# Performance work log

Measured on AMD Instinct MI355X. Metric: run time of the kernel, lower is better.

Reference implementation:

```python
import math
import jax, jax.numpy as jnp
import numpy as np

BS = 4; C = 128; D = 128; NH = 4; NL = 2; NP = 8
SHAPES = [(64, 96), (32, 48)]            # (H, W) per level
STARTS = [0, SHAPES[0][0] * SHAPES[0][1]]  # level_start_index


def lrelu(x):
    return jnp.where(x >= 0, x, 0.1 * x)


def conv2d(x, w, b):
    y = jax.lax.conv_general_dilated(x, w, (1, 1), [(1, 1), (1, 1)],
                                     dimension_numbers=('NCHW', 'OIHW', 'NCHW'))
    return y + b[None, :, None, None]


def pos_enc_sine(bs, H, W, npf=64, T=10000.0):
    # DETR PositionEmbeddingSine (normalize=True), mask of ones -> cumsum = index+1
    scale = 2.0 * math.pi
    eps = 1e-6
    y = (jnp.arange(1, H + 1, dtype=jnp.float32) / (H + eps) * scale)[:, None]
    x = (jnp.arange(1, W + 1, dtype=jnp.float32) / (W + eps) * scale)[None, :]
    y = jnp.broadcast_to(y, (H, W))
    x = jnp.broadcast_to(x, (H, W))
    dim_t = T ** (2.0 * (jnp.arange(npf) // 2).astype(jnp.float32) / npf)
    px = x[..., None] / dim_t
    py = y[..., None] / dim_t
    def interleave(p):
        return jnp.stack([jnp.sin(p[..., 0::2]), jnp.cos(p[..., 1::2])], -1).reshape(H, W, npf)
    pos = jnp.concatenate([interleave(py), interleave(px)], -1)  # [H,W,2*npf]
    return jnp.broadcast_to(pos.transpose(2, 0, 1)[None], (bs, 2 * npf, H, W))


def ref_points(bs, H, W):
    ys = (jnp.arange(H, dtype=jnp.float32) + 0.5) / H
    xs = (jnp.arange(W, dtype=jnp.float32) + 0.5) / W
    gy, gx = jnp.meshgrid(ys, xs, indexing='ij')
    ref = jnp.stack([gx.reshape(-1), gy.reshape(-1)], -1)  # [hw, 2] (x, y)
    return jnp.broadcast_to(ref[None, :, None, :], (bs, H * W, 1, 2))


def sample_level(v, loc, Hl, Wl):
    # v: [bs, Hl*Wl, nh, d]; loc: [bs, nq, nh, np, 2] in [0,1] -> grid_sample bilinear, zero pad
    bs, nq, nh, npts, _ = loc.shape
    d = v.shape[-1]
    x = loc[..., 0] * Wl - 0.5
    y = loc[..., 1] * Hl - 0.5
    x0f = jnp.floor(x); y0f = jnp.floor(y)
    fx = x - x0f; fy = y - y0f
    x0 = x0f.astype(jnp.int32); y0 = y0f.astype(jnp.int32)
    def gather(xi, yi):
        valid = (xi >= 0) & (xi < Wl) & (yi >= 0) & (yi < Hl)
        idx = jnp.clip(yi, 0, Hl - 1) * Wl + jnp.clip(xi, 0, Wl - 1)  # [bs,nq,nh,np]
        idx = idx.transpose(0, 1, 3, 2).reshape(bs, nq * npts, nh)
        g = jnp.take_along_axis(v, idx[..., None], axis=1)  # [bs,nq*np,nh,d]
        g = g.reshape(bs, nq, npts, nh, d).transpose(0, 1, 3, 2, 4)  # [bs,nq,nh,np,d]
        return g * valid[..., None]
    w00 = (1 - fx) * (1 - fy); w01 = fx * (1 - fy); w10 = (1 - fx) * fy; w11 = fx * fy
    return (gather(x0, y0) * w00[..., None] + gather(x0 + 1, y0) * w01[..., None]
            + gather(x0, y0 + 1) * w10[..., None] + gather(x0 + 1, y0 + 1) * w11[..., None])


def msda(value, loc, weights):
    # value [bs,Nv,nh,d], loc [bs,nq,nh,nl,np,2], weights [bs,nq,nh,nl,np]
    out = 0.0
    for l, (Hl, Wl) in enumerate(SHAPES):
        v_l = value[:, STARTS[l]:STARTS[l] + Hl * Wl]
        s = sample_level(v_l, loc[:, :, :, l], Hl, Wl)  # [bs,nq,nh,np,d]
        out = out + jnp.einsum('bqhpd,bqhp->bqhd', s, weights[:, :, :, l])
    bs, nq, nh, d = out.shape
    return out.reshape(bs, nq, nh * d)


def block(query, value, qloc, so_w, so_b, aw_w, aw_b, op_w, op_b):
    bs, nq, _ = query.shape
    off = (query @ so_w + so_b).reshape(bs, nq, NH, NL, NP, 2)
    aw = jax.nn.softmax((query @ aw_w + aw_b).reshape(bs, nq, NH, NL * NP), -1)
    aw = aw.reshape(bs, nq, NH, NL, NP)
    norm = jnp.array([[w, h] for (h, w) in SHAPES], jnp.float32)  # [nl,2] = (W,H)
    loc = qloc[:, :, None, :, None, :] + off / norm[None, None, None, :, None, :]
    return msda(value, loc, aw) @ op_w + op_b  # dropout = identity (eval)


def _forward(feat0_l0, feat0_l1, feat1_l0, feat1_l1,
             cw1, cb1, cw2, cb2, cw3, cb3, vw, vb, lvl_emb,
             so_w0, so_b0, aw_w0, aw_b0, op_w0, op_b0,
             so_w1, so_b1, aw_w1, aw_b1, op_w1, op_b1):
    bs = feat0_l0.shape[0]
    H1, W1 = SHAPES[-1]
    # scale_conv stem on feature0_list[-1]
    q = lrelu(conv2d(feat0_l1, cw1, cb1))
    q = lrelu(conv2d(q, cw2, cb2))
    q = lrelu(conv2d(q, cw3, cb3))
    q = q + pos_enc_sine(bs, H1, W1, npf=D // 2)
    qloc = ref_points(bs, H1, W1)  # [bs, hw, 1, 2]
    # flatten levels + level embeds
    f0 = jnp.concatenate([f.reshape(bs, C, -1) + lvl_emb[l][None, :, None]
                          for l, f in enumerate([feat0_l0, feat0_l1])], axis=2)
    f1 = jnp.concatenate([f.reshape(bs, C, -1) + lvl_emb[l][None, :, None]
                          for l, f in enumerate([feat1_l0, feat1_l1])], axis=2)
    cat = jnp.concatenate([f0, f1], axis=1)  # [bs, 2C, Nv]
    value = jnp.einsum('oc,bcn->bno', vw, cat) + vb  # 1x1 Conv1d -> [bs, Nv, D]
    value = jnp.broadcast_to(value[:, :, None, :], (bs, value.shape[1], NH, D))
    query = q.reshape(bs, D, -1).transpose(0, 2, 1)  # [bs, hw, D]
    query = block(query, value, qloc, so_w0, so_b0, aw_w0, aw_b0, op_w0, op_b0)
    query = block(query, value, qloc, so_w1, so_b1, aw_w1, aw_b1, op_w1, op_b1)
    return query.reshape(bs, H1, W1, D).transpose(0, 3, 1, 2)


def setup_inputs() -> dict:
    key = jax.random.key(0)
    ks = iter(jax.random.split(key, 32))
    def rn(shape, s=1.0):
        return jax.random.normal(next(ks), shape, jnp.float32) * s
    inp = {}
    inp['feat0_l0'] = rn((BS, C, SHAPES[0][0], SHAPES[0][1]))
    inp['feat0_l1'] = rn((BS, C, SHAPES[1][0], SHAPES[1][1]))
    inp['feat1_l0'] = rn((BS, C, SHAPES[0][0], SHAPES[0][1]))
    inp['feat1_l1'] = rn((BS, C, SHAPES[1][0], SHAPES[1][1]))
    inp['cw1'] = rn((2 * D, C, 3, 3), 0.03); inp['cb1'] = rn((2 * D,), 0.01)
    inp['cw2'] = rn((D, 2 * D, 3, 3), 0.03); inp['cb2'] = rn((D,), 0.01)
    inp['cw3'] = rn((D, D, 3, 3), 0.03); inp['cb3'] = rn((D,), 0.01)
    inp['vw'] = rn((D, 2 * C), 0.05); inp['vb'] = rn((D,), 0.01)
    inp['lvl_emb'] = rn((NL, C), 0.05)
    for i in range(2):
        inp[f'so_w{i}'] = rn((D, NH * NL * NP * 2), 0.02)
        inp[f'so_b{i}'] = rn((NH * NL * NP * 2,), 0.5)
        inp[f'aw_w{i}'] = rn((D, NH * NL * NP), 0.02)
        inp[f'aw_b{i}'] = rn((NH * NL * NP,), 0.01)
        inp[f'op_w{i}'] = rn((NH * D, D), 0.05)
        inp[f'op_b{i}'] = rn((D,), 0.01)
    return inp


def reference(feat0_l0, feat0_l1, feat1_l0, feat1_l1,
              cw1, cb1, cw2, cb2, cw3, cb3, vw, vb, lvl_emb,
              so_w0, so_b0, aw_w0, aw_b0, op_w0, op_b0,
              so_w1, so_b1, aw_w1, aw_b1, op_w1, op_b1):
    return _forward(feat0_l0, feat0_l1, feat1_l0, feat1_l1,
                    cw1, cb1, cw2, cb2, cw3, cb3, vw, vb, lvl_emb,
                    so_w0, so_b0, aw_w0, aw_b0, op_w0, op_b0,
                    so_w1, so_b1, aw_w1, aw_b1, op_w1, op_b1)
```

## Files before the change

kernel.cpp:

```cpp
#include <hip/hip_runtime.h>
#include <hip/hip_bf16.h>

typedef unsigned short u16;
typedef u16   u16x8 __attribute__((ext_vector_type(8)));
typedef short s16x8 __attribute__((ext_vector_type(8)));
typedef float f32x4 __attribute__((ext_vector_type(4)));

__device__ __forceinline__ float bf2f(u16 u) {
    union { unsigned int i; float f; } v; v.i = ((unsigned int)u) << 16; return v.f;
}
__device__ __forceinline__ u16 f2bf(float f) {
    unsigned int x = __float_as_uint(f);
    return (u16)((x + 0x7fffu + ((x >> 16) & 1u)) >> 16);
}
__device__ __forceinline__ float ldv(const void* p, size_t i, int f32) {
    return f32 ? ((const float*)p)[i] : bf2f(((const u16*)p)[i]);
}

template<int ACT, int OUTM, int OUT_BF16, int BN>
__device__ __forceinline__ void gemm_body(
    u16* __restrict__ smem, int bid,
    const u16* __restrict__ A, const u16* __restrict__ Bt,
    const u16* __restrict__ bias, void* __restrict__ Cv,
    int M, int K, int ldc, int nbase, const int* __restrict__ flag)
{
    constexpr int NF = BN >> 4;
    u16 (*As)[72] = (u16(*)[72])smem;
    u16 (*Bs)[72] = (u16(*)[72])(smem + 4608);

    const int t    = threadIdx.x;
    const int wv   = t >> 6, lane = t & 63;
    const int fr   = lane & 15, fg = lane >> 4;
    const int tiles_m = M >> 6;
    const int bm = bid % tiles_m, bn = bid / tiles_m;
    const int m0 = bm << 6, n0 = bn * BN;

    f32x4 acc[NF] = {};
    const int srow = t >> 2;
    const int scol = (t & 3) << 4;
    const int brow = (BN == 64) ? srow : (t >> 3);
    const int bcol = (BN == 64) ? scol : ((t & 7) << 3);
    const u16* Ap = A  + (size_t)(m0 + srow) * K + scol;
    const u16* Bp = Bt + (size_t)(n0 + brow) * K + bcol;

    const int ns = K >> 6;
    uint4 av0 = *(const uint4*)Ap, av1 = *(const uint4*)(Ap + 8);
    uint4 bv0 = *(const uint4*)Bp, bv1 = {0,0,0,0};
    if constexpr (BN == 64) bv1 = *(const uint4*)(Bp + 8);
    for (int s = 0; s < ns; ++s) {
        __syncthreads();
        *(uint4*)&As[srow][scol]     = av0;  *(uint4*)&As[srow][scol + 8] = av1;
        *(uint4*)&Bs[brow][bcol]     = bv0;
        if constexpr (BN == 64) *(uint4*)&Bs[brow][bcol + 8] = bv1;
        __syncthreads();
        if (s + 1 < ns) {
            const u16* An = Ap + ((s + 1) << 6);
            const u16* Bn = Bp + ((s + 1) << 6);
            av0 = *(const uint4*)An;  av1 = *(const uint4*)(An + 8);
            bv0 = *(const uint4*)Bn;
            if constexpr (BN == 64) bv1 = *(const uint4*)(Bn + 8);
        }
        union U { uint4 q; s16x8 v; };
        #pragma unroll
        for (int kk = 0; kk < 2; ++kk) {
            U af; af.q = *(const uint4*)&As[(wv << 4) + fr][(kk << 5) + (fg << 3)];
            U bf[NF];
            #pragma unroll
            for (int j = 0; j < NF; ++j)
                bf[j].q = *(const uint4*)&Bs[(j << 4) + fr][(kk << 5) + (fg << 3)];
            #pragma unroll
            for (int j = 0; j < NF; ++j)
                acc[j] = __builtin_amdgcn_mfma_f32_16x16x32_bf16(af.v, bf[j].v, acc[j], 0, 0, 0);
        }
    }

    float vv[NF][4];
    #pragma unroll
    for (int r = 0; r < 4; ++r) {
        float bvv = bf2f(bias[m0 + (wv << 4) + (fg << 2) + r]);
        #pragma unroll
        for (int j = 0; j < NF; ++j) {
            float v = acc[j][r] + bvv;
            if (ACT) v = (v >= 0.f) ? v : 0.1f * v;
            vv[j][r] = v;
        }
    }

    if constexpr (OUTM == 0) {
        #pragma unroll
        for (int j = 0; j < NF; ++j)
            #pragma unroll
            for (int r = 0; r < 4; ++r) {
                size_t idx = (size_t)(m0 + (wv << 4) + (fg << 2) + r) * ldc
                           + (nbase + n0 + (j << 4) + fr);
                if (OUT_BF16) ((u16*)Cv)[idx] = f2bf(vv[j][r]);
                else          ((float*)Cv)[idx] = vv[j][r];
            }
    } else if constexpr (OUTM == 1) {
        __syncthreads();
        u16* bb = smem;
        #pragma unroll
        for (int j = 0; j < NF; ++j)
            #pragma unroll
            for (int r = 0; r < 4; ++r)
                bb[((j << 4) + fr) * 72 + (wv << 4) + (fg << 2) + r] = f2bf(vv[j][r]);
        __syncthreads();
        if constexpr (BN == 64) {
            int row = t >> 2, seg = (t & 3) << 4;
            const uint4* src = (const uint4*)&bb[row * 72 + seg];
            uint4* dst = (uint4*)((u16*)Cv + (size_t)(nbase + n0 + row) * M + m0 + seg);
            dst[0] = src[0];
            dst[1] = src[1];
        } else {
            int row = t >> 3, seg = (t & 7) << 3;
            const uint4* src = (const uint4*)&bb[row * 72 + seg];
            uint4* dst = (uint4*)((u16*)Cv + (size_t)(nbase + n0 + row) * M + m0 + seg);
            dst[0] = src[0];
        }
    } else {
        __syncthreads();
        constexpr int LDB = BN + 8;
        u16* bb = smem;
        #pragma unroll
        for (int j = 0; j < NF; ++j)
            #pragma unroll
            for (int r = 0; r < 4; ++r)
                bb[((wv << 4) + (fg << 2) + r) * LDB + (j << 4) + fr] = f2bf(vv[j][r]);
        __syncthreads();
        int f32o = *flag;
        constexpr int EPT = BN / 4;
        int mrow = t >> 2, seg = (t & 3) * EPT;
        int b = n0 / 1536, hw0 = (n0 % 1536) + seg;
        size_t base = (size_t)(b * 128 + m0 + mrow) * 1536 + hw0;
        if (!f32o) {
            #pragma unroll
            for (int q = 0; q < EPT / 8; ++q)
                *(uint4*)((u16*)Cv + base + q * 8) = *(const uint4*)&bb[mrow * LDB + seg + q * 8];
        } else {
            float* dst = (float*)Cv + base;
            #pragma unroll
            for (int j = 0; j < EPT; ++j) dst[j] = bf2f(bb[mrow * LDB + seg + j]);
        }
    }
}

template<int CIN, int POS, int BN>
__device__ __forceinline__ void conv_body(
    u16* __restrict__ smem, int bid,
    const u16* __restrict__ A, const u16* __restrict__ X,
    const u16* __restrict__ bias, u16* __restrict__ Cv, int M)
{
    constexpr int NF = BN >> 4;
    u16 (*As)[72] = (u16(*)[72])smem;
    u16 (*Bs)[72] = (u16(*)[72])(smem + 4608);

    constexpr int NK2 = CIN / 64;
    constexpr int TOT = 9 * NK2;

    const int t    = threadIdx.x;
    const int wv   = t >> 6, lane = t & 63;
    const int fr   = lane & 15, fg = lane >> 4;
    const int tiles_m = M >> 6;
    const int bm = bid % tiles_m, bn = bid / tiles_m;
    const int m0 = bm << 6, n0 = bn * BN;

    const int srow = t >> 2;
    const int scol = (t & 3) << 4;
    const int brow = (BN == 64) ? srow : (t >> 3);
    const int bcol = (BN == 64) ? scol : ((t & 7) << 3);
    const int n  = n0 + brow;
    const int hw = n % 1536;
    const int hp = hw / 48, wp = hw % 48;
    const u16* Ar = A + (size_t)(m0 + srow) * (9 * CIN) + scol;

    f32x4 acc[NF] = {};

    auto ld = [&](int s, uint4& a0, uint4& a1, uint4& b0, uint4& b1) {
        int tap = s / NK2, k0 = (s % NK2) << 6;
        int dy = tap / 3 - 1, dx = tap % 3 - 1;
        bool vr = ((unsigned)(hp + dy) < 32u) && ((unsigned)(wp + dx) < 48u);
        const u16* Ap = Ar + tap * CIN + k0;
        a0 = *(const uint4*)Ap;  a1 = *(const uint4*)(Ap + 8);
        if (vr) {
            const u16* Bp = X + (size_t)(n + dy * 48 + dx) * CIN + bcol + k0;
            b0 = *(const uint4*)Bp;
            if constexpr (BN == 64) b1 = *(const uint4*)(Bp + 8);
        } else {
            b0 = uint4{0,0,0,0};  b1 = uint4{0,0,0,0};
        }
    };

    uint4 av0, av1, bv0, bv1;
    ld(0, av0, av1, bv0, bv1);
    for (int s = 0; s < TOT; ++s) {
        __syncthreads();
        *(uint4*)&As[srow][scol]     = av0;  *(uint4*)&As[srow][scol + 8] = av1;
        *(uint4*)&Bs[brow][bcol]     = bv0;
        if constexpr (BN == 64) *(uint4*)&Bs[brow][bcol + 8] = bv1;
        __syncthreads();
        if (s + 1 < TOT) ld(s + 1, av0, av1, bv0, bv1);
        union U { uint4 q; s16x8 v; };
        #pragma unroll
        for (int kk = 0; kk < 2; ++kk) {
            U af; af.q = *(const uint4*)&As[(wv << 4) + fr][(kk << 5) + (fg << 3)];
            U bf[NF];
            #pragma unroll
            for (int j = 0; j < NF; ++j)
                bf[j].q = *(const uint4*)&Bs[(j << 4) + fr][(kk << 5) + (fg << 3)];
            #pragma unroll
            for (int j = 0; j < NF; ++j)
                acc[j] = __builtin_amdgcn_mfma_f32_16x16x32_bf16(af.v, bf[j].v, acc[j], 0, 0, 0);
        }
    }

    float vv[NF][4];
    #pragma unroll
    for (int r = 0; r < 4; ++r) {
        float bvv = bf2f(bias[m0 + (wv << 4) + (fg << 2) + r]);
        #pragma unroll
        for (int j = 0; j < NF; ++j) {
            float v = acc[j][r] + bvv;
            vv[j][r] = (v >= 0.f) ? v : 0.1f * v;
        }
    }

    if (POS) {
        const float TWO_PI = 6.283185307179586f;
        #pragma unroll
        for (int j = 0; j < NF; ++j) {
            int ntok = n0 + (j << 4) + fr;
            int hw2 = ntok % 1536;
            int hp2 = hw2 / 48, wp2 = hw2 % 48;
            float yv = (float)(hp2 + 1) * (TWO_PI / (32.f + 1e-6f));
            float xv = (float)(wp2 + 1) * (TWO_PI / (48.f + 1e-6f));
            #pragma unroll
            for (int r = 0; r < 4; ++r) {
                int d = m0 + (wv << 4) + (fg << 2) + r;
                int mm = (d & 63) >> 1;
                float dim = exp2f((float)mm * (13.287712379549449f / 32.f));
                float val = ((d < 64) ? yv : xv) / dim;
                vv[j][r] += (d & 1) ? cosf(val) : sinf(val);
            }
        }
    }

    __syncthreads();
    u16* bb = smem;
    #pragma unroll
    for (int j = 0; j < NF; ++j)
        #pragma unroll
        for (int r = 0; r < 4; ++r)
            bb[((j << 4) + fr) * 72 + (wv << 4) + (fg << 2) + r] = f2bf(vv[j][r]);
    __syncthreads();
    if constexpr (BN == 64) {
        int row = t >> 2, seg = (t & 3) << 4;
        const uint4* src = (const uint4*)&bb[row * 72 + seg];
        uint4* dst = (uint4*)(Cv + (size_t)(n0 + row) * M + m0 + seg);
        dst[0] = src[0];
        dst[1] = src[1];
    } else {
        int row = t >> 3, seg = (t & 7) << 3;
        const uint4* src = (const uint4*)&bb[row * 72 + seg];
        uint4* dst = (uint4*)(Cv + (size_t)(n0 + row) * M + m0 + seg);
        dst[0] = src[0];
    }
}

template<int ACT, int OUTM, int OUT_BF16, int BN>
__global__ __launch_bounds__(256) void gemm_kn(
    const u16* __restrict__ A, const u16* __restrict__ Bt,
    const u16* __restrict__ bias, void* __restrict__ Cv,
    int M, int K, int ldc, int nbase, const int* __restrict__ flag)
{
    __shared__ __align__(16) u16 smem[9216];
    gemm_body<ACT, OUTM, OUT_BF16, BN>(smem, blockIdx.x, A, Bt, bias, Cv, M, K, ldc, nbase, flag);
}

template<int CIN, int POS, int BN>
__global__ __launch_bounds__(256) void conv_gemm(
    const u16* __restrict__ A, const u16* __restrict__ X,
    const u16* __restrict__ bias, u16* __restrict__ Cv, int M)
{
    __shared__ __align__(16) u16 smem[9216];
    conv_body<CIN, POS, BN>(smem, blockIdx.x, A, X, bias, Cv, M);
}

__global__ __launch_bounds__(256) void val_conv1_k(
    const u16* __restrict__ AVW, const u16* __restrict__ CATT,
    const u16* __restrict__ vb, u16* __restrict__ VAL,
    const u16* __restrict__ AW1, const u16* __restrict__ X0,
    const u16* __restrict__ cb1, u16* __restrict__ CH1)
{
    __shared__ __align__(16) u16 smem[9216];
    int bid = blockIdx.x;
    if (bid < 960) gemm_body<0, 1, 1, 64>(smem, bid, AVW, CATT, vb, VAL, 128, 256, 0, 0, nullptr);
    else           conv_body<128, 0, 64>(smem, bid - 960, AW1, X0, cb1, CH1, 256);
}

struct P21 { const void* p[21]; };

__global__ __launch_bounds__(256) void prep_fused(
    P21 a, const void* __restrict__ f00, const void* __restrict__ f01,
    const void* __restrict__ f10, const void* __restrict__ f11,
    int* __restrict__ FLAG,
    u16* AW1, u16* AW2, u16* AW3, u16* AVW,
    u16* APJ0, u16* APJ1, u16* AOP0, u16* AOP1,
    u16* BPJ0, u16* BPJ1, u16* SB,
    u16* CATT, u16* X0)
{
    __shared__ __align__(16) u16 Ts[128 * 66];
    const int t = threadIdx.x;
    unsigned int w = ((const unsigned int*)f00)[t];
    float pa = fabsf(bf2f((u16)(w & 0xFFFFu)));
    int cnt = __syncthreads_count(pa > 1e-6f && pa < 1e4f);
    const int f32 = (cnt < 128);
    const int bid = blockIdx.x;
    if (bid == 0 && t == 0) *FLAG = f32;

    if (bid < 3718) {
        int g = bid * 256 + t;
        if (g < 294912) { int m = g / 1152, rem = g % 1152, tap = rem >> 7, ci = rem & 127;
            AW1[g] = f2bf(ldv(a.p[0], (size_t)m * 1152 + ci * 9 + tap, f32)); return; }
        g -= 294912;
        if (g < 294912) { int m = g / 2304, rem = g % 2304, tap = rem >> 8, ci = rem & 255;
            AW2[g] = f2bf(ldv(a.p[2], (size_t)m * 2304 + ci * 9 + tap, f32)); return; }
        g -= 294912;
        if (g < 147456) { int m = g / 1152, rem = g % 1152, tap = rem >> 7, ci = rem & 127;
            AW3[g] = f2bf(ldv(a.p[4], (size_t)m * 1152 + ci * 9 + tap, f32)); return; }
        g -= 147456;
        if (g < 32768) { AVW[g] = f2bf(ldv(a.p[6], g, f32)); return; }
        g -= 32768;
        if (g < 24576) { int o = g >> 7, d = g & 127;
            APJ0[g] = f2bf(o < 128 ? ldv(a.p[9], d * 128 + o, f32)
                                   : ldv(a.p[11], d * 64 + (o - 128), f32)); return; }
        g -= 24576;
        if (g < 24576) { int o = g >> 7, d = g & 127;
            APJ1[g] = f2bf(o < 128 ? ldv(a.p[15], d * 128 + o, f32)
                                   : ldv(a.p[17], d * 64 + (o - 128), f32)); return; }
        g -= 24576;
        if (g < 65536) { int o = g >> 9, k = g & 511; AOP0[g] = f2bf(ldv(a.p[13], k * 128 + o, f32)); return; }
        g -= 65536;
        if (g < 65536) { int o = g >> 9, k = g & 511; AOP1[g] = f2bf(ldv(a.p[19], k * 128 + o, f32)); return; }
        g -= 65536;
        if (g < 192) { BPJ0[g] = f2bf(g < 128 ? ldv(a.p[10], g, f32) : ldv(a.p[12], g - 128, f32)); return; }
        g -= 192;
        if (g < 192) { BPJ1[g] = f2bf(g < 128 ? ldv(a.p[16], g, f32) : ldv(a.p[18], g - 128, f32)); return; }
        g -= 192;
        if (g < 1152) {
            const int off[8] = {0, 256, 384, 512, 640, 896, 1024, 1152};
            const int src[7] = {1, 3, 5, 7, 8, 14, 20};
            int s = 0;
            #pragma unroll
            for (int i = 1; i < 7; ++i) s += (g >= off[i]);
            SB[g] = f2bf(ldv(a.p[src[s]], g - off[s], f32));
        }
        return;
    }

    const void* src; u16* dst;
    int b, hw0, HW, rowlen, coloff, lvl, addemb;
    if (bid < 4678) {
        int g = bid - 3718;
        int half = g & 1;  g >>= 1;
        b = g / 120;  int tile = g % 120;
        lvl = (tile >= 96) ? 1 : 0;
        int tl = lvl ? tile - 96 : tile;
        hw0 = tl << 6;
        HW = lvl ? 1536 : 6144;
        src = (half == 0) ? (lvl ? f01 : f00) : (lvl ? f11 : f10);
        dst = CATT + (size_t)(b * 7680 + lvl * 6144 + hw0) * 256;
        rowlen = 256; coloff = half << 7; addemb = 1;
    } else {
        int g = bid - 4678;
        b = g / 24;  hw0 = (g % 24) << 6;
        HW = 1536; src = f01;
        dst = X0 + (size_t)(b * 1536 + hw0) * 128;
        rowlen = 128; coloff = 0; lvl = 1; addemb = 0;
    }

    {
        int c = t >> 1, hseg = (t & 1) << 5;
        size_t base = (size_t)(b * 128 + c) * HW + hw0 + hseg;
        u16* dstl = &Ts[c * 66 + hseg];
        if (!f32) {
            const u16* s8 = (const u16*)src + base;
            *(uint4*)(dstl)      = *(const uint4*)(s8);
            *(uint4*)(dstl + 8)  = *(const uint4*)(s8 + 8);
            *(uint4*)(dstl + 16) = *(const uint4*)(s8 + 16);
            *(uint4*)(dstl + 24) = *(const uint4*)(s8 + 24);
        } else {
            const float* sf = (const float*)src + base;
            #pragma unroll
            for (int q = 0; q < 32; ++q) dstl[q] = f2bf(sf[q]);
        }
    }
    __syncthreads();
    {
        int tok = t & 63, cseg = (t >> 6) << 5;
        u16 outv[32];
        #pragma unroll
        for (int j = 0; j < 32; ++j) {
            float x = bf2f(Ts[(cseg + j) * 66 + tok]);
            if (addemb) x += ldv(a.p[8], lvl * 128 + cseg + j, f32);
            outv[j] = f2bf(x);
        }
        u16* drow = dst + (size_t)tok * rowlen + coloff + cseg;
        #pragma unroll
        for (int q = 0; q < 4; ++q)
            *(uint4*)(drow + q * 8) = *(const uint4*)(&outv[q * 8]);
    }
}

__global__ void msda_sample(const float* __restrict__ PA, const u16* __restrict__ VAL,
                            u16* __restrict__ S)
{
    __shared__ int   SMI[4][64];
    __shared__ float SMW[4][64];
    __shared__ float LG[64];
    __shared__ float EW[64];
    int bid = blockIdx.x;
    int tok = ((bid & 7) * 768) + (bid >> 3);
    int t = threadIdx.x;
    int b = tok / 1536, hw = tok % 1536;
    int hp = hw / 48, wp = hw % 48;

    if (t < 64) {
        int l = (t >> 3) & 1, p = t & 7, h = t >> 4;
        int orow = h * 32 + l * 16 + p * 2;
        float offx = PA[(size_t)orow * 6144 + tok];
        float offy = PA[(size_t)(orow + 1) * 6144 + tok];
        LG[t]      = PA[(size_t)(128 + h * 16 + l * 8 + p) * 6144 + tok];
        float Wl = l ? 48.f : 96.f, Hl = l ? 32.f : 64.f;
        int iWl = l ? 48 : 96, iHl = l ? 32 : 64;
        int base = l ? 6144 : 0;
        float locx = (wp + 0.5f) / 48.f + offx / Wl;
        float locy = (hp + 0.5f) / 32.f + offy / Hl;
        float x = locx * Wl - 0.5f;
        float y = locy * Hl - 0.5f;
        float xf = floorf(x), yf = floorf(y);
        float fx = x - xf, fy = y - yf;
        int ix = (int)xf, iy = (int)yf;
        int vrow = b * 7680 + base;
        float w00 = (1.f - fx) * (1.f - fy), w01 = fx * (1.f - fy);
        float w10 = (1.f - fx) * fy,         w11 = fx * fy;
        bool vx0 = (ix >= 0) & (ix < iWl),     vx1 = (ix + 1 >= 0) & (ix + 1 < iWl);
        bool vy0 = (iy >= 0) & (iy < iHl),     vy1 = (iy + 1 >= 0) & (iy + 1 < iHl);
        SMI[0][t] = (vx0 & vy0) ? vrow + iy * iWl + ix           : 0;
        SMI[1][t] = (vx1 & vy0) ? vrow + iy * iWl + ix + 1       : 0;
        SMI[2][t] = (vx0 & vy1) ? vrow + (iy + 1) * iWl + ix     : 0;
        SMI[3][t] = (vx1 & vy1) ? vrow + (iy + 1) * iWl + ix + 1 : 0;
        SMW[0][t] = (vx0 & vy0) ? w00 : 0.f;
        SMW[1][t] = (vx1 & vy0) ? w01 : 0.f;
        SMW[2][t] = (vx0 & vy1) ? w10 : 0.f;
        SMW[3][t] = (vx1 & vy1) ? w11 : 0.f;
    }
    __syncthreads();
    if (t < 64) {
        int h0 = t & ~15;
        float mx = -1e30f;
        for (int i = 0; i < 16; ++i) mx = fmaxf(mx, LG[h0 + i]);
        EW[t] = expf(LG[t] - mx);
    }
    __syncthreads();
    if (t < 64) {
        int h0 = t & ~15;
        float s = 0.f;
        for (int i = 0; i < 16; ++i) s += EW[h0 + i];
        float aw = EW[t] / s;
        SMW[0][t] *= aw; SMW[1][t] *= aw; SMW[2][t] *= aw; SMW[3][t] *= aw;
    }
    __syncthreads();

    const int h = t >> 5, sub = t & 31, dseg = sub & 15, half = sub >> 4;
    const u16* Vb = VAL + (size_t)dseg * 8;
    float acc[8] = {0.f, 0.f, 0.f, 0.f, 0.f, 0.f, 0.f, 0.f};
    #pragma unroll
    for (int rr = 0; rr < 32; rr += 16) {
        u16x8 vreg[16];
        float wreg[16];
        #pragma unroll
        for (int q = 0; q < 16; ++q) {
            int pr = (half << 5) + rr + q;
            int s = pr >> 2, c = pr & 3;
            wreg[q] = SMW[c][(h << 4) + s];
            vreg[q] = *(const u16x8*)(Vb + (size_t)SMI[c][(h << 4) + s] * 128);
        }
        #pragma unroll
        for (int q = 0; q < 16; ++q)
            #pragma unroll
            for (int j = 0; j < 8; ++j) acc[j] += wreg[q] * bf2f(vreg[q][j]);
    }
    #pragma unroll
    for (int j = 0; j < 8; ++j) acc[j] += __shfl_xor(acc[j], 16, 64);
    if (!half) {
        u16x8 o;
        #pragma unroll
        for (int j = 0; j < 8; ++j) o[j] = f2bf(acc[j]);
        *(u16x8*)(S + (size_t)tok * 512 + (h << 7) + (dseg << 3)) = o;
    }
}

extern "C" void kernel_launch(void* const* d_in, const int* in_sizes, int n_in,
                              void* d_out, int out_size, void* d_ws, size_t ws_size,
                              hipStream_t stream)
{
    (void)in_sizes; (void)n_in; (void)out_size; (void)ws_size;

    char* ws = (char*)d_ws;
    size_t off = 0;
    auto alloc = [&](size_t bytes) { size_t o = off; off += (bytes + 255) & ~(size_t)255; return o; };
    int*   FLAG = (int*)(ws + alloc(256));
    u16*   AW1  = (u16*)(ws + alloc(294912ull * 2));
    u16*   AW2  = (u16*)(ws + alloc(294912ull * 2));
    u16*   AW3  = (u16*)(ws + alloc(147456ull * 2));
    u16*   AVW  = (u16*)(ws + alloc(32768ull * 2));
    u16*   APJ0 = (u16*)(ws + alloc(24576ull * 2));
    u16*   APJ1 = (u16*)(ws + alloc(24576ull * 2));
    u16*   AOP0 = (u16*)(ws + alloc(65536ull * 2));
    u16*   AOP1 = (u16*)(ws + alloc(65536ull * 2));
    u16*   BPJ0 = (u16*)(ws + alloc(512));
    u16*   BPJ1 = (u16*)(ws + alloc(512));
    u16*   SB   = (u16*)(ws + alloc(1152ull * 2));
    u16*   VAL  = (u16*)(ws + alloc(30720ull * 128 * 2));
    u16*   X0   = (u16*)(ws + alloc(6144ull * 128 * 2));
    u16*   CH1  = (u16*)(ws + alloc(6144ull * 256 * 2));
    u16*   CH2  = (u16*)(ws + alloc(6144ull * 128 * 2));
    u16*   QT0  = (u16*)(ws + alloc(6144ull * 128 * 2));
    u16*   QT1  = (u16*)(ws + alloc(6144ull * 128 * 2));
    char*  R    = ws + alloc(30720ull * 256 * 2);
    u16*   CATT = (u16*)R;
    float* PA   = (float*)R;
    u16*   S    = (u16*)(R + 192ull * 6144 * 4);

    u16* cb1C = SB + 0;   u16* cb2C = SB + 256;  u16* cb3C = SB + 384;
    u16* vbC  = SB + 512;
    u16* ob0C = SB + 896; u16* ob1C = SB + 1024;

    P21 a;
    const int widx[21] = {4,5,6,7,8,9,10,11,12, 13,14,15,16,17,18, 19,20,21,22,23,24};
    for (int i = 0; i < 21; ++i) a.p[i] = d_in[widx[i]];

    prep_fused<<<4774, 256, 0, stream>>>(a, d_in[0], d_in[1], d_in[2], d_in[3], FLAG,
                                         AW1, AW2, AW3, AVW,
                                         APJ0, APJ1, AOP0, AOP1, BPJ0, BPJ1, SB,
                                         CATT, X0);

    val_conv1_k<<<960 + 384, 256, 0, stream>>>(AVW, CATT, vbC, VAL, AW1, X0, cb1C, CH1);

    conv_gemm<256, 0, 32><<<2 * 192, 256, 0, stream>>>(AW2, CH1, cb2C, CH2, 128);
    conv_gemm<128, 1, 32><<<2 * 192, 256, 0, stream>>>(AW3, CH2, cb3C, QT0, 128);

    gemm_kn<0, 0, 0, 32><<<3 * 192, 256, 0, stream>>>(APJ0, QT0, BPJ0, PA, 192, 128, 6144, 0, FLAG);
    msda_sample<<<6144, 128, 0, stream>>>(PA, VAL, S);
    gemm_kn<0, 1, 1, 32><<<2 * 192, 256, 0, stream>>>(AOP0, S, ob0C, QT1, 128, 512, 0, 0, FLAG);

    gemm_kn<0, 0, 0, 32><<<3 * 192, 256, 0, stream>>>(APJ1, QT1, BPJ1, PA, 192, 128, 6144, 0, FLAG);
    msda_sample<<<6144, 128, 0, stream>>>(PA, VAL, S);
    gemm_kn<0, 2, 1, 32><<<2 * 192, 256, 0, stream>>>(AOP1, S, ob1C, d_out, 128, 512, 0, 0, FLAG);
}
```

Measured before the change: 143.6 us.

## Fuse sampling-offset projection, deformable sampling and output projection into one kernel

Replaces the three-kernel attention layer (projection GEMM to a global PA buffer, msda_sample, output-projection GEMM) with one kernel per layer that handles 16 tokens per block. The projection, softmax, bilinear sampling and output projection all run out of LDS. This removes the global round trips for PA and S and drops four kernel launches. In exchange each block re-reads the projection and output weights from global memory, only 384 blocks launch, and LDS use per block is large, which may lower occupancy for the latency-bound gather.

```diff
diff --git a/kernel.cpp b/kernel.cpp
--- a/kernel.cpp
+++ b/kernel.cpp
@@ -266,16 +266,6 @@
     }
 }
 
-template<int ACT, int OUTM, int OUT_BF16, int BN>
-__global__ __launch_bounds__(256) void gemm_kn(
-    const u16* __restrict__ A, const u16* __restrict__ Bt,
-    const u16* __restrict__ bias, void* __restrict__ Cv,
-    int M, int K, int ldc, int nbase, const int* __restrict__ flag)
-{
-    __shared__ __align__(16) u16 smem[9216];
-    gemm_body<ACT, OUTM, OUT_BF16, BN>(smem, blockIdx.x, A, Bt, bias, Cv, M, K, ldc, nbase, flag);
-}
-
 template<int CIN, int POS, int BN>
 __global__ __launch_bounds__(256) void conv_gemm(
     const u16* __restrict__ A, const u16* __restrict__ X,
@@ -295,6 +285,200 @@
     int bid = blockIdx.x;
     if (bid < 960) gemm_body<0, 1, 1, 64>(smem, bid, AVW, CATT, vb, VAL, 128, 256, 0, 0, nullptr);
     else           conv_body<128, 0, 64>(smem, bid - 960, AW1, X0, cb1, CH1, 256);
+}
+
+template<int OUTM>
+__global__ __launch_bounds__(256) void attn_fused(
+    const u16* __restrict__ QT, const u16* __restrict__ APJ,
+    const u16* __restrict__ BPJ, const u16* __restrict__ VAL,
+    const u16* __restrict__ AOP, const u16* __restrict__ OB,
+    void* __restrict__ OUT, const int* __restrict__ flag)
+{
+    __shared__ __align__(16) char lds[46144];
+    u16*   qs  = (u16*)lds;
+    u16*   Ss  = (u16*)(lds + 4352);
+    float* PAs = (float*)(lds + 20992);
+    float* XYs = (float*)(lds + 33856);
+    float* LGs = (float*)(lds + 42048);
+
+    const int t  = threadIdx.x;
+    const int wv = t >> 6, lane = t & 63;
+    const int fr = lane & 15, fg = lane >> 4;
+    const int bid = blockIdx.x;
+    const int tok0 = ((bid & 7) * 48 + (bid >> 3)) << 4;
+
+    union U { uint4 q; s16x8 v; };
+
+    {
+        int tok = t >> 4, seg = (t & 15) << 3;
+        *(uint4*)&qs[tok * 136 + seg] = *(const uint4*)&QT[(size_t)(tok0 + tok) * 128 + seg];
+    }
+    __syncthreads();
+
+    {
+        f32x4 pacc[3] = {};
+        #pragma unroll
+        for (int ks = 0; ks < 4; ++ks) {
+            U bf; bf.q = *(const uint4*)&qs[fr * 136 + ks * 32 + (fg << 3)];
+            #pragma unroll
+            for (int j = 0; j < 3; ++j) {
+                int m = ((wv * 3 + j) << 4) + fr;
+                U af; af.q = *(const uint4*)&APJ[(size_t)m * 128 + ks * 32 + (fg << 3)];
+                pacc[j] = __builtin_amdgcn_mfma_f32_16x16x32_bf16(af.v, bf.v, pacc[j], 0, 0, 0);
+            }
+        }
+        #pragma unroll
+        for (int j = 0; j < 3; ++j) {
+            int mb = (wv * 3 + j) << 4;
+            #pragma unroll
+            for (int r = 0; r < 4; ++r) {
+                int m = mb + (fg << 2) + r;
+                PAs[fr * 201 + m] = pacc[j][r] + bf2f(BPJ[m]);
+            }
+        }
+    }
+    __syncthreads();
+
+    #pragma unroll
+    for (int i = 0; i < 4; ++i) {
+        int slot = t + i * 256;
+        int tok = slot >> 6, s = slot & 63;
+        int h = s >> 4, l = (s >> 3) & 1, p = s & 7;
+        int orow = h * 32 + l * 16 + p * 2;
+        int lrow = 128 + h * 16 + l * 8 + p;
+        float offx = PAs[tok * 201 + orow];
+        float offy = PAs[tok * 201 + orow + 1];
+        int gtok = tok0 + tok;
+        int hw = gtok % 1536;
+        int hp = hw / 48, wp = hw % 48;
+        float Wl = l ? 48.f : 96.f, Hl = l ? 32.f : 64.f;
+        float locx = (wp + 0.5f) / 48.f + offx / Wl;
+        float locy = (hp + 0.5f) / 32.f + offy / Hl;
+        XYs[(tok * 64 + s) * 2]     = locx * Wl - 0.5f;
+        XYs[(tok * 64 + s) * 2 + 1] = locy * Hl - 0.5f;
+        LGs[tok * 64 + s] = PAs[tok * 201 + lrow];
+    }
+    __syncthreads();
+
+    float awr[4];
+    #pragma unroll
+    for (int i = 0; i < 4; ++i) {
+        int slot = t + i * 256;
+        int tok = slot >> 6, s = slot & 63;
+        const float* G = &LGs[tok * 64 + (s & ~15)];
+        float mx = -1e30f;
+        for (int j2 = 0; j2 < 16; ++j2) mx = fmaxf(mx, G[j2]);
+        float sum = 0.f;
+        for (int j2 = 0; j2 < 16; ++j2) sum += expf(G[j2] - mx);
+        awr[i] = expf(LGs[tok * 64 + s] - mx) / sum;
+    }
+    __syncthreads();
+    #pragma unroll
+    for (int i = 0; i < 4; ++i) {
+        int slot = t + i * 256;
+        LGs[(slot >> 6) * 64 + (slot & 63)] = awr[i];
+    }
+    __syncthreads();
+
+    {
+        const int tokg = t >> 5, sub = t & 31, h = sub >> 3, seg = sub & 7;
+        #pragma unroll
+        for (int round = 0; round < 2; ++round) {
+            int tok = round * 8 + tokg;
+            int b = (tok0 + tok) / 1536;
+            float acc[16];
+            #pragma unroll
+            for (int j = 0; j < 16; ++j) acc[j] = 0.f;
+            #pragma unroll 2
+            for (int s16i = 0; s16i < 16; ++s16i) {
+                int s = h * 16 + s16i;
+                int l = (s16i >> 3) & 1;
+                int iWl = l ? 48 : 96, iHl = l ? 32 : 64;
+                int vrow = b * 7680 + (l ? 6144 : 0);
+                float x  = XYs[(tok * 64 + s) * 2];
+                float y  = XYs[(tok * 64 + s) * 2 + 1];
+                float aw = LGs[tok * 64 + s];
+                float xf = floorf(x), yf = floorf(y);
+                float fx = x - xf, fy = y - yf;
+                int ix = (int)xf, iy = (int)yf;
+                bool vx0 = (unsigned)ix < (unsigned)iWl, vx1 = (unsigned)(ix + 1) < (unsigned)iWl;
+                bool vy0 = (unsigned)iy < (unsigned)iHl, vy1 = (unsigned)(iy + 1) < (unsigned)iHl;
+                float w0 = (vx0 && vy0) ? (1.f - fx) * (1.f - fy) * aw : 0.f;
+                float w1 = (vx1 && vy0) ? fx * (1.f - fy) * aw : 0.f;
+                float w2 = (vx0 && vy1) ? (1.f - fx) * fy * aw : 0.f;
+                float w3 = (vx1 && vy1) ? fx * fy * aw : 0.f;
+                int i0 = (vx0 && vy0) ? vrow + iy * iWl + ix           : 0;
+                int i1 = (vx1 && vy0) ? vrow + iy * iWl + ix + 1       : 0;
+                int i2 = (vx0 && vy1) ? vrow + (iy + 1) * iWl + ix     : 0;
+                int i3 = (vx1 && vy1) ? vrow + (iy + 1) * iWl + ix + 1 : 0;
+                const u16* p0 = VAL + (size_t)i0 * 128 + (seg << 4);
+                const u16* p1 = VAL + (size_t)i1 * 128 + (seg << 4);
+                const u16* p2 = VAL + (size_t)i2 * 128 + (seg << 4);
+                const u16* p3 = VAL + (size_t)i3 * 128 + (seg << 4);
+                u16x8 v0a = *(const u16x8*)p0, v0b = *(const u16x8*)(p0 + 8);
+                u16x8 v1a = *(const u16x8*)p1, v1b = *(const u16x8*)(p1 + 8);
+                u16x8 v2a = *(const u16x8*)p2, v2b = *(const u16x8*)(p2 + 8);
+                u16x8 v3a = *(const u16x8*)p3, v3b = *(const u16x8*)(p3 + 8);
+                #pragma unroll
+                for (int j = 0; j < 8; ++j) {
+                    acc[j]     += w0 * bf2f(v0a[j]) + w1 * bf2f(v1a[j])
+                                + w2 * bf2f(v2a[j]) + w3 * bf2f(v3a[j]);
+                    acc[8 + j] += w0 * bf2f(v0b[j]) + w1 * bf2f(v1b[j])
+                                + w2 * bf2f(v2b[j]) + w3 * bf2f(v3b[j]);
+                }
+            }
+            u16x8 o0, o1;
+            #pragma unroll
+            for (int j = 0; j < 8; ++j) { o0[j] = f2bf(acc[j]); o1[j] = f2bf(acc[8 + j]); }
+            u16* sp = &Ss[tok * 520 + (h << 7) + (seg << 4)];
+            *(u16x8*)sp = o0;
+            *(u16x8*)(sp + 8) = o1;
+        }
+    }
+    __syncthreads();
+
+    {
+        f32x4 oacc[2] = {};
+        for (int ks = 0; ks < 16; ++ks) {
+            U bf; bf.q = *(const uint4*)&Ss[fr * 520 + ks * 32 + (fg << 3)];
+            #pragma unroll
+            for (int j = 0; j < 2; ++j) {
+                int m = ((wv * 2 + j) << 4) + fr;
+                U af; af.q = *(const uint4*)&AOP[(size_t)m * 512 + ks * 32 + (fg << 3)];
+                oacc[j] = __builtin_amdgcn_mfma_f32_16x16x32_bf16(af.v, bf.v, oacc[j], 0, 0, 0);
+            }
+        }
+        #pragma unroll
+        for (int j = 0; j < 2; ++j) {
+            int mb = (wv * 2 + j) << 4;
+            #pragma unroll
+            for (int r = 0; r < 4; ++r) {
+                int m = mb + (fg << 2) + r;
+                qs[fr * 136 + m] = f2bf(oacc[j][r] + bf2f(OB[m]));
+            }
+        }
+    }
+    __syncthreads();
+
+    if constexpr (OUTM == 0) {
+        int tok = t >> 4, m0 = (t & 15) << 3;
+        *(uint4*)((u16*)OUT + (size_t)(tok0 + tok) * 128 + m0) = *(const uint4*)&qs[tok * 136 + m0];
+    } else {
+        int f32o = *flag;
+        int m = t & 127, grp = t >> 7;
+        int b = tok0 / 1536, hw0 = (tok0 % 1536) + (grp << 3);
+        size_t base = (size_t)(b * 128 + m) * 1536 + hw0;
+        if (!f32o) {
+            u16x8 o;
+            #pragma unroll
+            for (int j = 0; j < 8; ++j) o[j] = qs[((grp << 3) + j) * 136 + m];
+            *(u16x8*)((u16*)OUT + base) = o;
+        } else {
+            #pragma unroll
+            for (int j = 0; j < 8; ++j)
+                ((float*)OUT)[base + j] = bf2f(qs[((grp << 3) + j) * 136 + m]);
+        }
+    }
 }
 
 struct P21 { const void* p[21]; };
@@ -411,95 +595,6 @@
     }
 }
 
-__global__ void msda_sample(const float* __restrict__ PA, const u16* __restrict__ VAL,
-                            u16* __restrict__ S)
-{
-    __shared__ int   SMI[4][64];
-    __shared__ float SMW[4][64];
-    __shared__ float LG[64];
-    __shared__ float EW[64];
-    int bid = blockIdx.x;
-    int tok = ((bid & 7) * 768) + (bid >> 3);
-    int t = threadIdx.x;
-    int b = tok / 1536, hw = tok % 1536;
-    int hp = hw / 48, wp = hw % 48;
-
-    if (t < 64) {
-        int l = (t >> 3) & 1, p = t & 7, h = t >> 4;
-        int orow = h * 32 + l * 16 + p * 2;
-        float offx = PA[(size_t)orow * 6144 + tok];
-        float offy = PA[(size_t)(orow + 1) * 6144 + tok];
-        LG[t]      = PA[(size_t)(128 + h * 16 + l * 8 + p) * 6144 + tok];
-        float Wl = l ? 48.f : 96.f, Hl = l ? 32.f : 64.f;
-        int iWl = l ? 48 : 96, iHl = l ? 32 : 64;
-        int base = l ? 6144 : 0;
-        float locx = (wp + 0.5f) / 48.f + offx / Wl;
-        float locy = (hp + 0.5f) / 32.f + offy / Hl;
-        float x = locx * Wl - 0.5f;
-        float y = locy * Hl - 0.5f;
-        float xf = floorf(x), yf = floorf(y);
-        float fx = x - xf, fy = y - yf;
-        int ix = (int)xf, iy = (int)yf;
-        int vrow = b * 7680 + base;
-        float w00 = (1.f - fx) * (1.f - fy), w01 = fx * (1.f - fy);
-        float w10 = (1.f - fx) * fy,         w11 = fx * fy;
-        bool vx0 = (ix >= 0) & (ix < iWl),     vx1 = (ix + 1 >= 0) & (ix + 1 < iWl);
-        bool vy0 = (iy >= 0) & (iy < iHl),     vy1 = (iy + 1 >= 0) & (iy + 1 < iHl);
-        SMI[0][t] = (vx0 & vy0) ? vrow + iy * iWl + ix           : 0;
-        SMI[1][t] = (vx1 & vy0) ? vrow + iy * iWl + ix + 1       : 0;
-        SMI[2][t] = (vx0 & vy1) ? vrow + (iy + 1) * iWl + ix     : 0;
-        SMI[3][t] = (vx1 & vy1) ? vrow + (iy + 1) * iWl + ix + 1 : 0;
-        SMW[0][t] = (vx0 & vy0) ? w00 : 0.f;
-        SMW[1][t] = (vx1 & vy0) ? w01 : 0.f;
-        SMW[2][t] = (vx0 & vy1) ? w10 : 0.f;
-        SMW[3][t] = (vx1 & vy1) ? w11 : 0.f;
-    }
-    __syncthreads();
-    if (t < 64) {
-        int h0 = t & ~15;
-        float mx = -1e30f;
-        for (int i = 0; i < 16; ++i) mx = fmaxf(mx, LG[h0 + i]);
-        EW[t] = expf(LG[t] - mx);
-    }
-    __syncthreads();
-    if (t < 64) {
-        int h0 = t & ~15;
-        float s = 0.f;
-        for (int i = 0; i < 16; ++i) s += EW[h0 + i];
-        float aw = EW[t] / s;
-        SMW[0][t] *= aw; SMW[1][t] *= aw; SMW[2][t] *= aw; SMW[3][t] *= aw;
-    }
-    __syncthreads();
-
-    const int h = t >> 5, sub = t & 31, dseg = sub & 15, half = sub >> 4;
-    const u16* Vb = VAL + (size_t)dseg * 8;
-    float acc[8] = {0.f, 0.f, 0.f, 0.f, 0.f, 0.f, 0.f, 0.f};
-    #pragma unroll
-    for (int rr = 0; rr < 32; rr += 16) {
-        u16x8 vreg[16];
-        float wreg[16];
-        #pragma unroll
-        for (int q = 0; q < 16; ++q) {
-            int pr = (half << 5) + rr + q;
-            int s = pr >> 2, c = pr & 3;
-            wreg[q] = SMW[c][(h << 4) + s];
-            vreg[q] = *(const u16x8*)(Vb + (size_t)SMI[c][(h << 4) + s] * 128);
-        }
-        #pragma unroll
-        for (int q = 0; q < 16; ++q)
-            #pragma unroll
-            for (int j = 0; j < 8; ++j) acc[j] += wreg[q] * bf2f(vreg[q][j]);
-    }
-    #pragma unroll
-    for (int j = 0; j < 8; ++j) acc[j] += __shfl_xor(acc[j], 16, 64);
-    if (!half) {
-        u16x8 o;
-        #pragma unroll
-        for (int j = 0; j < 8; ++j) o[j] = f2bf(acc[j]);
-        *(u16x8*)(S + (size_t)tok * 512 + (h << 7) + (dseg << 3)) = o;
-    }
-}
-
 extern "C" void kernel_launch(void* const* d_in, const int* in_sizes, int n_in,
                               void* d_out, int out_size, void* d_ws, size_t ws_size,
                               hipStream_t stream)
@@ -527,10 +622,7 @@
     u16*   CH2  = (u16*)(ws + alloc(6144ull * 128 * 2));
     u16*   QT0  = (u16*)(ws + alloc(6144ull * 128 * 2));
     u16*   QT1  = (u16*)(ws + alloc(6144ull * 128 * 2));
-    char*  R    = ws + alloc(30720ull * 256 * 2);
-    u16*   CATT = (u16*)R;
-    float* PA   = (float*)R;
-    u16*   S    = (u16*)(R + 192ull * 6144 * 4);
+    u16*   CATT = (u16*)(ws + alloc(30720ull * 256 * 2));
 
     u16* cb1C = SB + 0;   u16* cb2C = SB + 256;  u16* cb3C = SB + 384;
     u16* vbC  = SB + 512;
@@ -550,11 +642,7 @@
     conv_gemm<256, 0, 32><<<2 * 192, 256, 0, stream>>>(AW2, CH1, cb2C, CH2, 128);
     conv_gemm<128, 1, 32><<<2 * 192, 256, 0, stream>>>(AW3, CH2, cb3C, QT0, 128);
 
-    gemm_kn<0, 0, 0, 32><<<3 * 192, 256, 0, stream>>>(APJ0, QT0, BPJ0, PA, 192, 128, 6144, 0, FLAG);
-    msda_sample<<<6144, 128, 0, stream>>>(PA, VAL, S);
-    gemm_kn<0, 1, 1, 32><<<2 * 192, 256, 0, stream>>>(AOP0, S, ob0C, QT1, 128, 512, 0, 0, FLAG);
-
-    gemm_kn<0, 0, 0, 32><<<3 * 192, 256, 0, stream>>>(APJ1, QT1, BPJ1, PA, 192, 128, 6144, 0, FLAG);
-    msda_sample<<<6144, 128, 0, stream>>>(PA, VAL, S);
-    gemm_kn<0, 2, 1, 32><<<2 * 192, 256, 0, stream>>>(AOP1, S, ob1C, d_out, 128, 512, 0, 0, FLAG);
-}
+    attn_fused<0><<<384, 256, 0, stream>>>(QT0, APJ0, BPJ0, VAL, AOP0, ob0C, QT1, FLAG);
+
+    attn_fused<1><<<384, 256, 0, stream>>>(QT1, APJ1, BPJ1, VAL, AOP1, ob1C, d_out, FLAG);
+}
```

Result: slower. 152.6 us (+6.3%).

## Fuse offset/attention projection GEMM into deformable-attention sampling kernel

Applied to the files above, without the earlier changes.

Replaces the separate projection GEMM (writing fp32 PA to global) plus sampling kernel with one kernel. Each 512-thread block computes the 192-wide projection for 4 tokens via MFMA into shared memory, then does the softmax, bilinear index setup and value gathering for those tokens. This removes a launch and the global round trip of the PA buffer. In exchange, the MFMA is padded from 4 to 16 columns, so three quarters of that work is wasted, and APJ is re-read by every block.

```diff
diff --git a/kernel.cpp b/kernel.cpp
--- a/kernel.cpp
+++ b/kernel.cpp
@@ -295,6 +295,144 @@
     int bid = blockIdx.x;
     if (bid < 960) gemm_body<0, 1, 1, 64>(smem, bid, AVW, CATT, vb, VAL, 128, 256, 0, 0, nullptr);
     else           conv_body<128, 0, 64>(smem, bid - 960, AW1, X0, cb1, CH1, 256);
+}
+
+__global__ __launch_bounds__(512) void msda_proj(
+    const u16* __restrict__ QT, const u16* __restrict__ APJ,
+    const u16* __restrict__ BPJ, const u16* __restrict__ VAL,
+    u16* __restrict__ S)
+{
+    __shared__ __align__(16) u16 qs[16 * 136];
+    __shared__ float PAs[4][201];
+    __shared__ int   SMI[4][256];
+    __shared__ float SMW[4][256];
+    __shared__ float LG[256];
+    __shared__ float EW[256];
+
+    const int t  = threadIdx.x;
+    const int wv = t >> 6, lane = t & 63;
+    const int fr = lane & 15, fg = lane >> 4;
+    const int bid = blockIdx.x;
+    const int tok0 = ((bid & 7) * 192 + (bid >> 3)) << 2;
+
+    union U { uint4 q; s16x8 v; };
+
+    if (t < 256) {
+        int tok = t >> 4, seg = (t & 15) << 3;
+        uint4 v = {0, 0, 0, 0};
+        if (tok < 4) v = *(const uint4*)&QT[(size_t)(tok0 + tok) * 128 + seg];
+        *(uint4*)&qs[tok * 136 + seg] = v;
+    }
+    __syncthreads();
+
+    if (wv < 6) {
+        f32x4 pacc[2] = {};
+        #pragma unroll
+        for (int ks = 0; ks < 4; ++ks) {
+            U bf; bf.q = *(const uint4*)&qs[fr * 136 + ks * 32 + (fg << 3)];
+            #pragma unroll
+            for (int j = 0; j < 2; ++j) {
+                int m = ((wv * 2 + j) << 4) + fr;
+                U af; af.q = *(const uint4*)&APJ[(size_t)m * 128 + ks * 32 + (fg << 3)];
+                pacc[j] = __builtin_amdgcn_mfma_f32_16x16x32_bf16(af.v, bf.v, pacc[j], 0, 0, 0);
+            }
+        }
+        if (fr < 4) {
+            #pragma unroll
+            for (int j = 0; j < 2; ++j) {
+                int mb = (wv * 2 + j) << 4;
+                #pragma unroll
+                for (int r = 0; r < 4; ++r) {
+                    int m = mb + (fg << 2) + r;
+                    PAs[fr][m] = pacc[j][r] + bf2f(BPJ[m]);
+                }
+            }
+        }
+    }
+    __syncthreads();
+
+    if (t < 256) {
+        int tok = t >> 6, s = t & 63;
+        int h = s >> 4, l = (s >> 3) & 1, p = s & 7;
+        int orow = h * 32 + l * 16 + p * 2;
+        float offx = PAs[tok][orow];
+        float offy = PAs[tok][orow + 1];
+        LG[t] = PAs[tok][128 + h * 16 + l * 8 + p];
+        int gtok = tok0 + tok;
+        int b = gtok / 1536, hw = gtok % 1536;
+        int hp = hw / 48, wp = hw % 48;
+        float Wl = l ? 48.f : 96.f, Hl = l ? 32.f : 64.f;
+        int iWl = l ? 48 : 96, iHl = l ? 32 : 64;
+        int base = l ? 6144 : 0;
+        float locx = (wp + 0.5f) / 48.f + offx / Wl;
+        float locy = (hp + 0.5f) / 32.f + offy / Hl;
+        float x = locx * Wl - 0.5f;
+        float y = locy * Hl - 0.5f;
+        float xf = floorf(x), yf = floorf(y);
+        float fx = x - xf, fy = y - yf;
+        int ix = (int)xf, iy = (int)yf;
+        int vrow = b * 7680 + base;
+        float w00 = (1.f - fx) * (1.f - fy), w01 = fx * (1.f - fy);
+        float w10 = (1.f - fx) * fy,         w11 = fx * fy;
+        bool vx0 = (unsigned)ix < (unsigned)iWl,       vx1 = (unsigned)(ix + 1) < (unsigned)iWl;
+        bool vy0 = (unsigned)iy < (unsigned)iHl,       vy1 = (unsigned)(iy + 1) < (unsigned)iHl;
+        SMI[0][t] = (vx0 && vy0) ? vrow + iy * iWl + ix           : 0;
+        SMI[1][t] = (vx1 && vy0) ? vrow + iy * iWl + ix + 1       : 0;
+        SMI[2][t] = (vx0 && vy1) ? vrow + (iy + 1) * iWl + ix     : 0;
+        SMI[3][t] = (vx1 && vy1) ? vrow + (iy + 1) * iWl + ix + 1 : 0;
+        SMW[0][t] = (vx0 && vy0) ? w00 : 0.f;
+        SMW[1][t] = (vx1 && vy0) ? w01 : 0.f;
+        SMW[2][t] = (vx0 && vy1) ? w10 : 0.f;
+        SMW[3][t] = (vx1 && vy1) ? w11 : 0.f;
+    }
+    __syncthreads();
+    if (t < 256) {
+        int h0 = t & ~15;
+        float mx = -1e30f;
+        for (int i = 0; i < 16; ++i) mx = fmaxf(mx, LG[h0 + i]);
+        EW[t] = expf(LG[t] - mx);
+    }
+    __syncthreads();
+    if (t < 256) {
+        int h0 = t & ~15;
+        float sum = 0.f;
+        for (int i = 0; i < 16; ++i) sum += EW[h0 + i];
+        float aw = EW[t] / sum;
+        SMW[0][t] *= aw; SMW[1][t] *= aw; SMW[2][t] *= aw; SMW[3][t] *= aw;
+    }
+    __syncthreads();
+
+    {
+        const int tok = t >> 7, sub = t & 127;
+        const int h = sub >> 5, subsub = sub & 31, dseg = subsub & 15, half = subsub >> 4;
+        const int smbase = (tok << 6) + (h << 4);
+        const u16* Vb = VAL + (size_t)dseg * 8;
+        float acc[8] = {0.f, 0.f, 0.f, 0.f, 0.f, 0.f, 0.f, 0.f};
+        #pragma unroll
+        for (int rr = 0; rr < 32; rr += 16) {
+            u16x8 vreg[16];
+            float wreg[16];
+            #pragma unroll
+            for (int q = 0; q < 16; ++q) {
+                int pr = (half << 5) + rr + q;
+                int s = pr >> 2, c = pr & 3;
+                wreg[q] = SMW[c][smbase + s];
+                vreg[q] = *(const u16x8*)(Vb + (size_t)SMI[c][smbase + s] * 128);
+            }
+            #pragma unroll
+            for (int q = 0; q < 16; ++q)
+                #pragma unroll
+                for (int j = 0; j < 8; ++j) acc[j] += wreg[q] * bf2f(vreg[q][j]);
+        }
+        #pragma unroll
+        for (int j = 0; j < 8; ++j) acc[j] += __shfl_xor(acc[j], 16, 64);
+        if (!half) {
+            u16x8 o;
+            #pragma unroll
+            for (int j = 0; j < 8; ++j) o[j] = f2bf(acc[j]);
+            *(u16x8*)(S + (size_t)(tok0 + tok) * 512 + (h << 7) + (dseg << 3)) = o;
+        }
+    }
 }
 
 struct P21 { const void* p[21]; };
@@ -411,95 +549,6 @@
     }
 }
 
-__global__ void msda_sample(const float* __restrict__ PA, const u16* __restrict__ VAL,
-                            u16* __restrict__ S)
-{
-    __shared__ int   SMI[4][64];
-    __shared__ float SMW[4][64];
-    __shared__ float LG[64];
-    __shared__ float EW[64];
-    int bid = blockIdx.x;
-    int tok = ((bid & 7) * 768) + (bid >> 3);
-    int t = threadIdx.x;
-    int b = tok / 1536, hw = tok % 1536;
-    int hp = hw / 48, wp = hw % 48;
-
-    if (t < 64) {
-        int l = (t >> 3) & 1, p = t & 7, h = t >> 4;
-        int orow = h * 32 + l * 16 + p * 2;
-        float offx = PA[(size_t)orow * 6144 + tok];
-        float offy = PA[(size_t)(orow + 1) * 6144 + tok];
-        LG[t]      = PA[(size_t)(128 + h * 16 + l * 8 + p) * 6144 + tok];
-        float Wl = l ? 48.f : 96.f, Hl = l ? 32.f : 64.f;
-        int iWl = l ? 48 : 96, iHl = l ? 32 : 64;
-        int base = l ? 6144 : 0;
-        float locx = (wp + 0.5f) / 48.f + offx / Wl;
-        float locy = (hp + 0.5f) / 32.f + offy / Hl;
-        float x = locx * Wl - 0.5f;
-        float y = locy * Hl - 0.5f;
-        float xf = floorf(x), yf = floorf(y);
-        float fx = x - xf, fy = y - yf;
-        int ix = (int)xf, iy = (int)yf;
-        int vrow = b * 7680 + base;
-        float w00 = (1.f - fx) * (1.f - fy), w01 = fx * (1.f - fy);
-        float w10 = (1.f - fx) * fy,         w11 = fx * fy;
-        bool vx0 = (ix >= 0) & (ix < iWl),     vx1 = (ix + 1 >= 0) & (ix + 1 < iWl);
-        bool vy0 = (iy >= 0) & (iy < iHl),     vy1 = (iy + 1 >= 0) & (iy + 1 < iHl);
-        SMI[0][t] = (vx0 & vy0) ? vrow + iy * iWl + ix           : 0;
-        SMI[1][t] = (vx1 & vy0) ? vrow + iy * iWl + ix + 1       : 0;
-        SMI[2][t] = (vx0 & vy1) ? vrow + (iy + 1) * iWl + ix     : 0;
-        SMI[3][t] = (vx1 & vy1) ? vrow + (iy + 1) * iWl + ix + 1 : 0;
-        SMW[0][t] = (vx0 & vy0) ? w00 : 0.f;
-        SMW[1][t] = (vx1 & vy0) ? w01 : 0.f;
-        SMW[2][t] = (vx0 & vy1) ? w10 : 0.f;
-        SMW[3][t] = (vx1 & vy1) ? w11 : 0.f;
-    }
-    __syncthreads();
-    if (t < 64) {
-        int h0 = t & ~15;
-        float mx = -1e30f;
-        for (int i = 0; i < 16; ++i) mx = fmaxf(mx, LG[h0 + i]);
-        EW[t] = expf(LG[t] - mx);
-    }
-    __syncthreads();
-    if (t < 64) {
-        int h0 = t & ~15;
-        float s = 0.f;
-        for (int i = 0; i < 16; ++i) s += EW[h0 + i];
-        float aw = EW[t] / s;
-        SMW[0][t] *= aw; SMW[1][t] *= aw; SMW[2][t] *= aw; SMW[3][t] *= aw;
-    }
-    __syncthreads();
-
-    const int h = t >> 5, sub = t & 31, dseg = sub & 15, half = sub >> 4;
-    const u16* Vb = VAL + (size_t)dseg * 8;
-    float acc[8] = {0.f, 0.f, 0.f, 0.f, 0.f, 0.f, 0.f, 0.f};
-    #pragma unroll
-    for (int rr = 0; rr < 32; rr += 16) {
-        u16x8 vreg[16];
-        float wreg[16];
-        #pragma unroll
-        for (int q = 0; q < 16; ++q) {
-            int pr = (half << 5) + rr + q;
-            int s = pr >> 2, c = pr & 3;
-            wreg[q] = SMW[c][(h << 4) + s];
-            vreg[q] = *(const u16x8*)(Vb + (size_t)SMI[c][(h << 4) + s] * 128);
-        }
-        #pragma unroll
-        for (int q = 0; q < 16; ++q)
-            #pragma unroll
-            for (int j = 0; j < 8; ++j) acc[j] += wreg[q] * bf2f(vreg[q][j]);
-    }
-    #pragma unroll
-    for (int j = 0; j < 8; ++j) acc[j] += __shfl_xor(acc[j], 16, 64);
-    if (!half) {
-        u16x8 o;
-        #pragma unroll
-        for (int j = 0; j < 8; ++j) o[j] = f2bf(acc[j]);
-        *(u16x8*)(S + (size_t)tok * 512 + (h << 7) + (dseg << 3)) = o;
-    }
-}
-
 extern "C" void kernel_launch(void* const* d_in, const int* in_sizes, int n_in,
                               void* d_out, int out_size, void* d_ws, size_t ws_size,
                               hipStream_t stream)
@@ -529,8 +578,7 @@
     u16*   QT1  = (u16*)(ws + alloc(6144ull * 128 * 2));
     char*  R    = ws + alloc(30720ull * 256 * 2);
     u16*   CATT = (u16*)R;
-    float* PA   = (float*)R;
-    u16*   S    = (u16*)(R + 192ull * 6144 * 4);
+    u16*   S    = (u16*)R;
 
     u16* cb1C = SB + 0;   u16* cb2C = SB + 256;  u16* cb3C = SB + 384;
     u16* vbC  = SB + 512;
@@ -550,11 +598,9 @@
     conv_gemm<256, 0, 32><<<2 * 192, 256, 0, stream>>>(AW2, CH1, cb2C, CH2, 128);
     conv_gemm<128, 1, 32><<<2 * 192, 256, 0, stream>>>(AW3, CH2, cb3C, QT0, 128);
 
-    gemm_kn<0, 0, 0, 32><<<3 * 192, 256, 0, stream>>>(APJ0, QT0, BPJ0, PA, 192, 128, 6144, 0, FLAG);
-    msda_sample<<<6144, 128, 0, stream>>>(PA, VAL, S);
+    msda_proj<<<1536, 512, 0, stream>>>(QT0, APJ0, BPJ0, VAL, S);
     gemm_kn<0, 1, 1, 32><<<2 * 192, 256, 0, stream>>>(AOP0, S, ob0C, QT1, 128, 512, 0, 0, FLAG);
 
-    gemm_kn<0, 0, 0, 32><<<3 * 192, 256, 0, stream>>>(APJ1, QT1, BPJ1, PA, 192, 128, 6144, 0, FLAG);
-    msda_sample<<<6144, 128, 0, stream>>>(PA, VAL, S);
+    msda_proj<<<1536, 512, 0, stream>>>(QT1, APJ1, BPJ1, VAL, S);
     gemm_kn<0, 2, 1, 32><<<2 * 192, 256, 0, stream>>>(AOP1, S, ob1C, d_out, 128, 512, 0, 0, FLAG);
 }
```

Result: slower. 149.8 us (+4.3%).
